# Performance work log

Hardware: AMD Instinct MI355X
Metric: run time of the kernel (lower is better)

Reference implementation:

```python
import jax, jax.numpy as jnp
import numpy as np

DIM = 2048
N_EXPERTS = 16
TOP_K = 4
MOE_INTER = 1024
SHARED_INTER = 2 * MOE_INTER  # n_shared_experts * moe_inter_dim
B, S = 4, 1024
INIT = 0.02


def setup_inputs() -> dict:
    key = jax.random.key(0)
    ks = jax.random.split(key, 8)
    return {
        "x": jax.random.normal(ks[0], (B, S, DIM), dtype=jnp.float32),
        "gate_w": jax.random.normal(ks[1], (DIM, N_EXPERTS), dtype=jnp.float32) * INIT,
        "w1": jax.random.normal(ks[2], (N_EXPERTS, DIM, MOE_INTER), dtype=jnp.float32) * INIT,
        "w2": jax.random.normal(ks[3], (N_EXPERTS, MOE_INTER, DIM), dtype=jnp.float32) * INIT,
        "w3": jax.random.normal(ks[4], (N_EXPERTS, DIM, MOE_INTER), dtype=jnp.float32) * INIT,
        "ws1": jax.random.normal(ks[5], (DIM, SHARED_INTER), dtype=jnp.float32) * INIT,
        "ws2": jax.random.normal(ks[6], (SHARED_INTER, DIM), dtype=jnp.float32) * INIT,
        "ws3": jax.random.normal(ks[7], (DIM, SHARED_INTER), dtype=jnp.float32) * INIT,
    }


def _moe_forward(x, gate_w, w1, w2, w3, ws1, ws2, ws3):
    shape = x.shape
    xf = x.reshape(-1, DIM)  # [T, D]
    # Gate: softmax scores, top-k selection (weights are the top-k probs)
    scores = jax.nn.softmax(xf @ gate_w, axis=-1)          # [T, E]
    weights, indices = jax.lax.top_k(scores, TOP_K)         # [T, K] each
    y = jnp.zeros_like(xf)
    # Fixed loop over experts (structural, not over data dims).
    for e in range(N_EXPERTS):
        # gate coefficient for expert e: 0 if not in token's top-k
        coef = jnp.sum(weights * (indices == e), axis=-1)   # [T]
        h = jax.nn.silu(xf @ w1[e]) * (xf @ w3[e])          # [T, I]
        y = y + coef[:, None] * (h @ w2[e])
    # Shared experts (always-on gated MLP)
    z = (jax.nn.silu(xf @ ws1) * (xf @ ws3)) @ ws2
    return (y + z).reshape(shape)


def reference(x, gate_w, w1, w2, w3, ws1, ws2, ws3):
    return _moe_forward(x, gate_w, w1, w2, w3, ws1, ws2, ws3)
```

## Files before the change

kernel.cpp:

```cpp
#include <hip/hip_runtime.h>
#include <hip/hip_bf16.h>
#include <stdint.h>

#define T_TOK 4096
#define DIMD  2048
#define NEXP  16
#define TOPK  4
#define NI    1024
#define NSH   2048
#define TCAP  320

typedef __attribute__((ext_vector_type(8))) short short8;
typedef __attribute__((ext_vector_type(4))) float f32x4;
typedef __attribute__((ext_vector_type(4))) unsigned short u16x4;
typedef __attribute__((ext_vector_type(8))) unsigned short u16x8;

__device__ __forceinline__ unsigned short f2bf(float f) {
    union { float f; unsigned u; } v; v.f = f;
    return (unsigned short)((v.u + 0x7fffu + ((v.u >> 16) & 1u)) >> 16);
}

__device__ __forceinline__ float bf2f(unsigned short b) {
    union { unsigned u; float f; } v; v.u = (unsigned)b << 16;
    return v.f;
}

__device__ __forceinline__ void gload16(const void* g, void* l) {
    __builtin_amdgcn_global_load_lds(
        (const __attribute__((address_space(1))) void*)g,
        (__attribute__((address_space(3))) void*)l, 16, 0, 0);
}

__global__ __launch_bounds__(256) void gwt_kernel(const float* __restrict__ gw,
                                                  float* __restrict__ gwT) {
    int i = blockIdx.x * 256 + threadIdx.x;
    int d = i >> 4, e = i & 15;
    gwT[e * DIMD + d] = gw[i];
}

__global__ __launch_bounds__(256) void gate_kernel(const float* __restrict__ x,
                                                   const float* __restrict__ gwT,
                                                   int* __restrict__ blk_cnt,
                                                   int* __restrict__ tk_er,
                                                   float* __restrict__ tk_wv,
                                                   unsigned short* __restrict__ xb) {
    __shared__ int h[16];
    const int blk = blockIdx.x;
    const int t = blk * 4 + (threadIdx.x >> 6);
    const int lane = threadIdx.x & 63;
    if (threadIdx.x < 16) h[threadIdx.x] = 0;
    __syncthreads();

    const f32x4* xr = (const f32x4*)(x + (size_t)t * DIMD);
    f32x4 xv[8];
#pragma unroll
    for (int i = 0; i < 8; ++i) xv[i] = xr[i * 64 + lane];

    {
        unsigned short* xo = xb + (size_t)t * DIMD;
#pragma unroll
        for (int i = 0; i < 8; ++i) {
            u16x4 o;
#pragma unroll
            for (int j = 0; j < 4; ++j) o[j] = f2bf(xv[i][j]);
            *(u16x4*)(xo + i * 256 + lane * 4) = o;
        }
    }

    float acc[NEXP];
#pragma unroll
    for (int e = 0; e < NEXP; ++e) {
        const f32x4* gr = (const f32x4*)(gwT + e * DIMD);
        float s = 0.f;
#pragma unroll
        for (int i = 0; i < 8; ++i) {
            f32x4 gv = gr[i * 64 + lane];
            s += xv[i][0] * gv[0] + xv[i][1] * gv[1] +
                 xv[i][2] * gv[2] + xv[i][3] * gv[3];
        }
        acc[e] = s;
    }
#pragma unroll
    for (int e = 0; e < NEXP; ++e) {
        float v = acc[e];
#pragma unroll
        for (int off = 32; off; off >>= 1) v += __shfl_xor(v, off, 64);
        acc[e] = v;
    }
    float m = acc[0];
#pragma unroll
    for (int e = 1; e < NEXP; ++e) m = fmaxf(m, acc[e]);
    float s = 0.f;
#pragma unroll
    for (int e = 0; e < NEXP; ++e) { acc[e] = expf(acc[e] - m); s += acc[e]; }
    float inv = 1.f / s;
#pragma unroll
    for (int e = 0; e < NEXP; ++e) acc[e] *= inv;

    float w4[TOPK]; int i4[TOPK];
#pragma unroll
    for (int k = 0; k < TOPK; ++k) {
        float bv = -1.f; int be = 0;
#pragma unroll
        for (int e = 0; e < NEXP; ++e)
            if (acc[e] > bv) { bv = acc[e]; be = e; }
        w4[k] = bv; i4[k] = be;
#pragma unroll
        for (int e = 0; e < NEXP; ++e)
            if (e == be) acc[e] = -1.f;
    }

    if (lane == 0) {
        int r4[TOPK];
#pragma unroll
        for (int k = 0; k < TOPK; ++k) r4[k] = atomicAdd(&h[i4[k]], 1);
#pragma unroll
        for (int k = 0; k < TOPK; ++k) {
            tk_er[t * 4 + k] = (i4[k] << 20) | r4[k];
            tk_wv[t * 4 + k] = w4[k];
        }
    }
    __syncthreads();
    if (threadIdx.x < 16) blk_cnt[blk * 16 + threadIdx.x] = h[threadIdx.x];
}

__global__ __launch_bounds__(256) void scan_kernel(const int* __restrict__ blk_cnt,
                                                   int* __restrict__ blk_off,
                                                   int* __restrict__ cnt,
                                                   int* __restrict__ offs,
                                                   int* __restrict__ table) {
    __shared__ int gsum[16][17];
    __shared__ int gbase[16][17];
    __shared__ int csh[16];
    int tid = threadIdx.x;
    int e = tid >> 4, g = tid & 15;
    {
        int s = 0;
        for (int b = g * 64; b < g * 64 + 64; ++b) s += blk_cnt[b * 16 + e];
        gsum[e][g] = s;
    }
    __syncthreads();
    if (tid < 16) {
        int run = 0;
        for (int g2 = 0; g2 < 16; ++g2) { gbase[tid][g2] = run; run += gsum[tid][g2]; }
        csh[tid] = run;
        cnt[tid] = run;
    }
    __syncthreads();
    {
        int run = gbase[e][g];
        for (int b = g * 64; b < g * 64 + 64; ++b) {
            blk_off[b * 16 + e] = run;
            run += blk_cnt[b * 16 + e];
        }
    }
    if (tid == 0) {
        int o = 0;
        for (int e2 = 0; e2 < 16; ++e2) { offs[e2] = o; o += csh[e2]; }
        offs[NEXP] = o;
    }
    __syncthreads();
    for (int idx = tid; idx < 8 * TCAP; idx += 256) {
        int c = idx & 7, j = idx >> 3;
        int n0 = ((csh[c] + 127) >> 7) << 3;
        int n1 = ((csh[c + 8] + 127) >> 7) << 3;
        int v = -1;
        if (j < n0)
            v = (c << 16) | ((j & 7) << 13) | ((j >> 3) * 128);
        else if (j < n0 + n1) {
            int j2 = j - n0;
            v = ((c + 8) << 16) | ((j2 & 7) << 13) | ((j2 >> 3) * 128);
        }
        table[idx] = v;
    }
}

__global__ __launch_bounds__(256) void fill_kernel(const int* __restrict__ tk_er,
                                                   const float* __restrict__ tk_wv,
                                                   const int* __restrict__ blk_off,
                                                   const int* __restrict__ offs,
                                                   int* __restrict__ list,
                                                   float* __restrict__ cw,
                                                   int* __restrict__ rows) {
    int i = blockIdx.x * 256 + threadIdx.x;
    int rec = tk_er[i];
    int e = rec >> 20, r = rec & 0xFFFFF;
    int t = i >> 2;
    int ro = blk_off[(t >> 2) * 16 + e] + r;
    list[e * T_TOK + ro] = t;
    cw[e * T_TOK + ro] = tk_wv[i];
    rows[i] = offs[e] + ro;
}

__global__ __launch_bounds__(256) void tq_pair(const float* __restrict__ s1,
                                               const float* __restrict__ s3,
                                               unsigned short* __restrict__ dst,
                                               int K, int N,
                                               size_t srcStrideE, size_t dstStrideE) {
    int e = blockIdx.z;
    s1 += (size_t)e * srcStrideE;
    s3 += (size_t)e * srcStrideE;
    dst += (size_t)e * dstStrideE;
    __shared__ unsigned short tile[64][72];
    const int t = threadIdx.x;
    const int k0 = blockIdx.y * 64, n0 = blockIdx.x * 64;
    const int lr = t >> 4, lc4 = (t & 15) * 4;
    const int sr8 = (t & 7) * 8, sn = t >> 3;
#pragma unroll
    for (int half = 0; half < 2; ++half) {
        const float* src = half ? s3 : s1;
#pragma unroll
        for (int r = 0; r < 4; ++r) {
            f32x4 v = *(const f32x4*)(src + (size_t)(k0 + lr + r * 16) * N + n0 + lc4);
#pragma unroll
            for (int j = 0; j < 4; ++j) tile[lr + r * 16][lc4 + j] = f2bf(v[j]);
        }
        __syncthreads();
#pragma unroll
        for (int q = 0; q < 2; ++q) {
            int nn = sn + q * 32;
            int n = n0 + nn;
            int rrow = (n >> 4) * 32 + half * 16 + (n & 15);
            u16x8 o;
#pragma unroll
            for (int j = 0; j < 8; ++j) o[j] = tile[sr8 + j][nn];
            *(u16x8*)(dst + (size_t)rrow * K + k0 + sr8) = o;
        }
        __syncthreads();
    }
}

__global__ __launch_bounds__(256) void tq_plain(const float* __restrict__ src,
                                                unsigned short* __restrict__ dst,
                                                int K, int N,
                                                size_t srcStrideE, size_t dstStrideE) {
    int e = blockIdx.z;
    src += (size_t)e * srcStrideE;
    dst += (size_t)e * dstStrideE;
    __shared__ unsigned short tile[64][72];
    const int t = threadIdx.x;
    const int k0 = blockIdx.y * 64, n0 = blockIdx.x * 64;
    const int lr = t >> 4, lc4 = (t & 15) * 4;
    const int sr8 = (t & 7) * 8, sn = t >> 3;
#pragma unroll
    for (int r = 0; r < 4; ++r) {
        f32x4 v = *(const f32x4*)(src + (size_t)(k0 + lr + r * 16) * N + n0 + lc4);
#pragma unroll
        for (int j = 0; j < 4; ++j) tile[lr + r * 16][lc4 + j] = f2bf(v[j]);
    }
    __syncthreads();
#pragma unroll
    for (int q = 0; q < 2; ++q) {
        int nn = sn + q * 32;
        int n = n0 + nn;
        u16x8 o;
#pragma unroll
        for (int j = 0; j < 8; ++j) o[j] = tile[sr8 + j][nn];
        *(u16x8*)(dst + (size_t)n * K + k0 + sr8) = o;
    }
}

__global__ __launch_bounds__(256) void gather_kernel(const unsigned short* __restrict__ dbuf,
                                                     const int* __restrict__ rows,
                                                     float* __restrict__ out) {
    const int t = blockIdx.x;
    const int c8 = threadIdx.x * 8;
    int r[4];
#pragma unroll
    for (int k = 0; k < 4; ++k) r[k] = rows[t * 4 + k];
    f32x4 a0, a1;
    {
        const f32x4* z = (const f32x4*)(out + (size_t)t * DIMD + c8);
        a0 = z[0]; a1 = z[1];
    }
#pragma unroll
    for (int k = 0; k < 4; ++k) {
        u16x8 d = *(const u16x8*)(dbuf + (size_t)r[k] * DIMD + c8);
#pragma unroll
        for (int j = 0; j < 4; ++j) { a0[j] += bf2f(d[j]); a1[j] += bf2f(d[4 + j]); }
    }
    f32x4* o = (f32x4*)(out + (size_t)t * DIMD + c8);
    o[0] = a0; o[1] = a1;
}

template <bool UP>
__global__ __launch_bounds__(512, 2) void gemm_f(
    const unsigned short* __restrict__ Ash, const unsigned short* __restrict__ Art,
    const unsigned short* __restrict__ Bsh, const unsigned short* __restrict__ Brt,
    const int* __restrict__ cnt, const int* __restrict__ offs,
    const int* __restrict__ list, const float* __restrict__ cw,
    unsigned short* __restrict__ hs, unsigned short* __restrict__ hbuf,
    float* __restrict__ fout, unsigned short* __restrict__ dbuf,
    const int* __restrict__ table) {
    constexpr int SHBLK = UP ? 512 : 256;

    const int bid = blockIdx.x;
    const bool routed = bid >= SHBLK;
    int bx, rb, e = 0, M, obase = 0;
    const unsigned short* Ap;
    const unsigned short* Bp;
    int ASTRr, BSTRr;
    if (!routed) {
        if (UP) { bx = bid & 15; rb = (bid >> 4) * 128; }
        else    { bx = bid >> 5; rb = (bid & 31) * 128; }
        M = T_TOK;
        Ap = Ash; Bp = Bsh;
        ASTRr = 2048; BSTRr = 2048;
    } else {
        int pk = table[bid - SHBLK];
        if (pk < 0) return;
        e = pk >> 16; bx = (pk >> 13) & 7; rb = pk & 8191;
        M = cnt[e]; obase = offs[e];
        Ap = Art;
        Bp = Brt + (UP ? (size_t)e * 2048 * 2048 : (size_t)e * 2048 * 1024);
        ASTRr = UP ? 2048 : 1024;
        BSTRr = UP ? 2048 : 1024;
    }
    const int NT = (!UP && routed) ? 32 : 64;

    extern __shared__ char smem[];

    const int tid = threadIdx.x;
    const int lane = tid & 63, wid = tid >> 6;
    const int wm = wid >> 2, wn = wid & 3;
    const int fr = lane & 15, fq = lane >> 4;
    const int offR = ((fr >> 1) << 7) + (((((fr & 1) << 2) | fq) ^ (fr >> 1)) << 4);
    const int d16 = tid * 16;

    const unsigned short* pA;
    const unsigned short* pB0;
    const unsigned short* pB1;
    {
        int c = tid, s = c >> 3, sl = (c & 7) ^ (s & 7);
        int rA = 2 * s + (sl >> 2), kk = (sl & 3) * 8;
        int gr = rb + rA;
        int cr = (gr < M) ? gr : (M - 1);
        size_t arow;
        if (!routed)  arow = (size_t)gr;
        else if (UP)  arow = (size_t)list[e * T_TOK + cr];
        else          arow = (size_t)(obase + cr);
        pA = Ap + arow * ASTRr + kk;
    }
#pragma unroll
    for (int u = 0; u < 2; ++u) {
        int c = u * 512 + tid, s = c >> 3, sl = (c & 7) ^ (s & 7);
        int rB = 2 * s + (sl >> 2), kk = (sl & 3) * 8;
        const unsigned short* p = Bp + (size_t)(bx * 256 + rB) * BSTRr + kk;
        if (u == 0) pB0 = p; else pB1 = p;
    }

    f32x4 acc[4][4];
#pragma unroll
    for (int m = 0; m < 4; ++m)
#pragma unroll
        for (int n = 0; n < 4; ++n) acc[m][n] = (f32x4)0.f;

    gload16(pA,      (void*)(smem + 0 + d16));
    gload16(pA + 32, (void*)(smem + 8192 + d16));
    gload16(pB0,      (void*)(smem + 24576 + d16));
    gload16(pB1,      (void*)(smem + 24576 + 8192 + d16));
    gload16(pB0 + 32, (void*)(smem + 24576 + 16384 + d16));
    gload16(pB1 + 32, (void*)(smem + 24576 + 16384 + 8192 + d16));
    pA += 64; pB0 += 64; pB1 += 64;
    asm volatile("s_waitcnt vmcnt(0)" ::: "memory");
    __builtin_amdgcn_s_barrier();

    int bA = 0, bA2 = 16384;
    int bB = 0, bB2 = 32768;
    for (int t = 0; t < NT; ++t) {
        short8 aF[4], bF[4];
#pragma unroll
        for (int m = 0; m < 4; ++m)
            aF[m] = *(const short8*)(smem + bA + wm * 4096 + m * 1024 + offR);
#pragma unroll
        for (int n = 0; n < 4; ++n)
            bF[n] = *(const short8*)(smem + 24576 + bB + wn * 4096 + n * 1024 + offR);
        const bool more = (t + 2 < NT);
        if (more) {
            gload16(pA, (void*)(smem + bA2 + d16));
            gload16(pB0, (void*)(smem + 24576 + bB2 + d16));
            gload16(pB1, (void*)(smem + 24576 + bB2 + 8192 + d16));
            pA += 32; pB0 += 32; pB1 += 32;
        }
        __builtin_amdgcn_s_setprio(1);
#pragma unroll
        for (int m = 0; m < 4; ++m)
#pragma unroll
            for (int n = 0; n < 4; ++n)
                acc[m][n] = __builtin_amdgcn_mfma_f32_16x16x32_bf16(aF[m], bF[n], acc[m][n], 0, 0, 0);
        __builtin_amdgcn_s_setprio(0);
        if (more) { asm volatile("s_waitcnt vmcnt(3)" ::: "memory"); }
        else      { asm volatile("s_waitcnt vmcnt(0)" ::: "memory"); }
        __builtin_amdgcn_s_barrier();
        bA = (bA == 16384) ? 0 : bA + 8192;
        bA2 = (bA2 == 16384) ? 0 : bA2 + 8192;
        bB = (bB == 32768) ? 0 : bB + 16384;
        bB2 = (bB2 == 32768) ? 0 : bB2 + 16384;
    }

    if constexpr (UP) {
        const int LDO = routed ? NI : NSH;
        unsigned short* hp = routed ? hbuf : hs;
#pragma unroll
        for (int m = 0; m < 4; ++m)
#pragma unroll
            for (int q = 0; q < 4; ++q) {
                int gr = rb + wm * 64 + m * 16 + fq * 4 + q;
                if (gr < M) {
                    float coef = routed ? cw[e * T_TOK + gr] : 1.f;
                    size_t orow = (size_t)((routed ? obase : 0) + gr) * LDO;
#pragma unroll
                    for (int nfp = 0; nfp < 2; ++nfp) {
                        float c1 = acc[m][2 * nfp][q], c3 = acc[m][2 * nfp + 1][q];
                        float h = c1 / (1.f + __expf(-c1)) * c3 * coef;
                        int ncol = (bx * 8 + wn * 2 + nfp) * 16 + fr;
                        hp[orow + ncol] = f2bf(h);
                    }
                }
            }
    } else {
#pragma unroll
        for (int m = 0; m < 4; ++m)
#pragma unroll
            for (int q = 0; q < 4; ++q) {
                int gr = rb + wm * 64 + m * 16 + fq * 4 + q;
                if (gr < M) {
                    if (routed) {
                        unsigned short* op = dbuf + (size_t)(obase + gr) * DIMD;
#pragma unroll
                        for (int nf = 0; nf < 4; ++nf) {
                            int col = bx * 256 + wn * 64 + nf * 16 + fr;
                            op[col] = f2bf(acc[m][nf][q]);
                        }
                    } else {
                        float* op = fout + (size_t)gr * DIMD;
#pragma unroll
                        for (int nf = 0; nf < 4; ++nf) {
                            int col = bx * 256 + wn * 64 + nf * 16 + fr;
                            op[col] = acc[m][nf][q];
                        }
                    }
                }
            }
    }
}

extern "C" void kernel_launch(void* const* d_in, const int* in_sizes, int n_in,
                              void* d_out, int out_size, void* d_ws, size_t ws_size,
                              hipStream_t stream) {
    const float* x   = (const float*)d_in[0];
    const float* gw  = (const float*)d_in[1];
    const float* w1  = (const float*)d_in[2];
    const float* w2  = (const float*)d_in[3];
    const float* w3  = (const float*)d_in[4];
    const float* ws1 = (const float*)d_in[5];
    const float* ws2 = (const float*)d_in[6];
    const float* ws3 = (const float*)d_in[7];
    float* out = (float*)d_out;

    char* p = (char*)d_ws;
    unsigned short* xb   = (unsigned short*)p; p += (size_t)T_TOK * DIMD * 2;
    unsigned short* hs   = (unsigned short*)p; p += (size_t)T_TOK * NSH * 2;
    unsigned short* hbuf = (unsigned short*)p; p += (size_t)T_TOK * TOPK * NI * 2;
    unsigned short* upT  = (unsigned short*)p; p += (size_t)NEXP * 2048 * DIMD * 2;
    unsigned short* w2T  = (unsigned short*)p; p += (size_t)NEXP * DIMD * NI * 2;
    unsigned short* upsT = (unsigned short*)p; p += (size_t)2 * NSH * DIMD * 2;
    unsigned short* ws2T = (unsigned short*)p; p += (size_t)DIMD * NSH * 2;
    float* gwT = (float*)p;                    p += (size_t)NEXP * DIMD * 4;
    float* cw = (float*)p;                     p += (size_t)NEXP * T_TOK * 4;
    int* list = (int*)p;                       p += (size_t)NEXP * T_TOK * 4;
    int* tk_er = (int*)p;                      p += (size_t)T_TOK * TOPK * 4;
    float* tk_wv = (float*)p;                  p += (size_t)T_TOK * TOPK * 4;
    int* rows = (int*)p;                       p += (size_t)T_TOK * TOPK * 4;
    int* blk_cnt = (int*)p;                    p += (size_t)1024 * 16 * 4;
    int* blk_off = (int*)p;                    p += (size_t)1024 * 16 * 4;
    int* cnt = (int*)p;                        p += 256;
    int* offs = (int*)p;                       p += 256;
    int* table = (int*)p;                      p += 4096 * 4;
    if ((size_t)(p - (char*)d_ws) > ws_size) return;
    unsigned short* dbuf = upT;

    hipFuncSetAttribute((const void*)&gemm_f<true>, hipFuncAttributeMaxDynamicSharedMemorySize, 73728);
    hipFuncSetAttribute((const void*)&gemm_f<false>, hipFuncAttributeMaxDynamicSharedMemorySize, 73728);

    gwt_kernel<<<(NEXP * DIMD) / 256, 256, 0, stream>>>(gw, gwT);
    gate_kernel<<<T_TOK / 4, 256, 0, stream>>>(x, gwT, blk_cnt, tk_er, tk_wv, xb);
    scan_kernel<<<1, 256, 0, stream>>>(blk_cnt, blk_off, cnt, offs, table);
    fill_kernel<<<T_TOK * TOPK / 256, 256, 0, stream>>>(tk_er, tk_wv, blk_off, offs,
                                                        list, cw, rows);

    tq_pair<<<dim3(NI / 64, DIMD / 64, NEXP), 256, 0, stream>>>(
        w1, w3, upT, DIMD, NI, (size_t)DIMD * NI, (size_t)2048 * DIMD);
    tq_pair<<<dim3(NSH / 64, DIMD / 64, 1), 256, 0, stream>>>(
        ws1, ws3, upsT, DIMD, NSH, 0, 0);
    tq_plain<<<dim3(DIMD / 64, NI / 64, NEXP), 256, 0, stream>>>(
        w2, w2T, NI, DIMD, (size_t)NI * DIMD, (size_t)DIMD * NI);
    tq_plain<<<dim3(DIMD / 64, NSH / 64, 1), 256, 0, stream>>>(
        ws2, ws2T, NSH, DIMD, 0, 0);

    gemm_f<true><<<512 + 8 * TCAP, 512, 73728, stream>>>(
        xb, xb, upsT, upT, cnt, offs, list, cw, hs, hbuf, nullptr, nullptr, table);
    gemm_f<false><<<256 + 8 * TCAP, 512, 73728, stream>>>(
        hs, hbuf, ws2T, w2T, cnt, offs, list, nullptr, nullptr, nullptr, out, dbuf, table);
    gather_kernel<<<T_TOK, 256, 0, stream>>>(dbuf, rows, out);
}
```

Before: 591.3 us.

## Enlarge GEMM tiles to 256x256 with K=64 steps and interleaved quadrant pipeline

Rewrites the fused grouped GEMM to compute 256x256 output tiles per block with a 64-wide K step, double-buffered in 128 KB of LDS. The main loop is split into four quadrant MFMA phases, with LDS reads and global-to-LDS loads interleaved between barriers. The routed tile table and block counts are rescaled to match. The goal is more data reuse per byte loaded and fewer blocks. The cost is one block per CU, more padding waste on small per-expert row counts, and more barriers per iteration.

```diff
diff --git a/kernel.cpp b/kernel.cpp
--- a/kernel.cpp
+++ b/kernel.cpp
@@ -8,7 +8,7 @@
 #define TOPK  4
 #define NI    1024
 #define NSH   2048
-#define TCAP  320
+#define TCAP  256
 
 typedef __attribute__((ext_vector_type(8))) short short8;
 typedef __attribute__((ext_vector_type(4))) float f32x4;
@@ -162,14 +162,14 @@
     __syncthreads();
     for (int idx = tid; idx < 8 * TCAP; idx += 256) {
         int c = idx & 7, j = idx >> 3;
-        int n0 = ((csh[c] + 127) >> 7) << 3;
-        int n1 = ((csh[c + 8] + 127) >> 7) << 3;
+        int n0 = ((csh[c] + 255) >> 8) << 3;
+        int n1 = ((csh[c + 8] + 255) >> 8) << 3;
         int v = -1;
         if (j < n0)
-            v = (c << 16) | ((j & 7) << 13) | ((j >> 3) * 128);
+            v = (c << 16) | ((j & 7) << 13) | ((j >> 3) * 256);
         else if (j < n0 + n1) {
             int j2 = j - n0;
-            v = ((c + 8) << 16) | ((j2 & 7) << 13) | ((j2 >> 3) * 128);
+            v = ((c + 8) << 16) | ((j2 & 7) << 13) | ((j2 >> 3) * 256);
         }
         table[idx] = v;
     }
@@ -283,6 +283,51 @@
     o[0] = a0; o[1] = a1;
 }
 
+
+#define BAR __builtin_amdgcn_s_barrier()
+#define LGKM0 do { asm volatile("s_waitcnt lgkmcnt(0)" ::: "memory"); \
+                   __builtin_amdgcn_sched_barrier(0); } while (0)
+
+#define SA(H, D, KT) do { \
+    gload16(pA[H][0] + (KT) * 64, (void*)(smem + (D) * 32768 + dofs[H][0])); \
+    gload16(pA[H][1] + (KT) * 64, (void*)(smem + (D) * 32768 + dofs[H][1])); \
+  } while (0)
+#define SB(H, D, KT) do { \
+    gload16(pB[H][0] + (KT) * 64, (void*)(smem + 65536 + (D) * 32768 + dofs[H][0])); \
+    gload16(pB[H][1] + (KT) * 64, (void*)(smem + 65536 + (D) * 32768 + dofs[H][1])); \
+  } while (0)
+
+#define RDA(MH, D) do { \
+    _Pragma("unroll") \
+    for (int m2 = 0; m2 < 4; ++m2) { \
+      const char* bp = smem + (D) * 32768 + wm * 16384 + ((MH) * 64 + m2 * 16 + fr) * 128; \
+      aF[m2][0] = *(const short8*)(bp + kA0); \
+      aF[m2][1] = *(const short8*)(bp + kA1); \
+    } } while (0)
+#define RDB(dst, NH, D) do { \
+    _Pragma("unroll") \
+    for (int n2 = 0; n2 < 2; ++n2) { \
+      const char* bp = smem + 65536 + (D) * 32768 + (wn >> 1) * 16384 + \
+                       ((wn & 1) * 64 + (NH) * 32 + n2 * 16 + fr) * 128; \
+      dst[n2][0] = *(const short8*)(bp + kA0); \
+      dst[n2][1] = *(const short8*)(bp + kA1); \
+    } } while (0)
+
+#define MM(MH, NH, BF) do { \
+    __builtin_amdgcn_s_setprio(1); \
+    _Pragma("unroll") \
+    for (int m2 = 0; m2 < 4; ++m2) { \
+      _Pragma("unroll") \
+      for (int n2 = 0; n2 < 2; ++n2) { \
+        acc[(MH) * 4 + m2][(NH) * 2 + n2] = __builtin_amdgcn_mfma_f32_16x16x32_bf16( \
+            aF[m2][0], BF[n2][0], acc[(MH) * 4 + m2][(NH) * 2 + n2], 0, 0, 0); \
+        acc[(MH) * 4 + m2][(NH) * 2 + n2] = __builtin_amdgcn_mfma_f32_16x16x32_bf16( \
+            aF[m2][1], BF[n2][1], acc[(MH) * 4 + m2][(NH) * 2 + n2], 0, 0, 0); \
+      } \
+    } \
+    __builtin_amdgcn_s_setprio(0); \
+  } while (0)
+
 template <bool UP>
 __global__ __launch_bounds__(512, 2) void gemm_f(
     const unsigned short* __restrict__ Ash, const unsigned short* __restrict__ Art,
@@ -292,7 +337,7 @@
     unsigned short* __restrict__ hs, unsigned short* __restrict__ hbuf,
     float* __restrict__ fout, unsigned short* __restrict__ dbuf,
     const int* __restrict__ table) {
-    constexpr int SHBLK = UP ? 512 : 256;
+    constexpr int SHBLK = UP ? 256 : 128;
 
     const int bid = blockIdx.x;
     const bool routed = bid >= SHBLK;
@@ -301,8 +346,8 @@
     const unsigned short* Bp;
     int ASTRr, BSTRr;
     if (!routed) {
-        if (UP) { bx = bid & 15; rb = (bid >> 4) * 128; }
-        else    { bx = bid >> 5; rb = (bid & 31) * 128; }
+        if (UP) { bx = bid & 15; rb = (bid >> 4) * 256; }
+        else    { bx = bid >> 4; rb = (bid & 15) * 256; }
         M = T_TOK;
         Ap = Ash; Bp = Bsh;
         ASTRr = 2048; BSTRr = 2048;
@@ -316,7 +361,7 @@
         ASTRr = UP ? 2048 : 1024;
         BSTRr = UP ? 2048 : 1024;
     }
-    const int NT = (!UP && routed) ? 32 : 64;
+    const int NT = UP ? 32 : (routed ? 16 : 32);
 
     extern __shared__ char smem[];
 
@@ -324,120 +369,111 @@
     const int lane = tid & 63, wid = tid >> 6;
     const int wm = wid >> 2, wn = wid & 3;
     const int fr = lane & 15, fq = lane >> 4;
-    const int offR = ((fr >> 1) << 7) + (((((fr & 1) << 2) | fq) ^ (fr >> 1)) << 4);
-    const int d16 = tid * 16;
-
-    const unsigned short* pA;
-    const unsigned short* pB0;
-    const unsigned short* pB1;
-    {
-        int c = tid, s = c >> 3, sl = (c & 7) ^ (s & 7);
-        int rA = 2 * s + (sl >> 2), kk = (sl & 3) * 8;
-        int gr = rb + rA;
-        int cr = (gr < M) ? gr : (M - 1);
-        size_t arow;
-        if (!routed)  arow = (size_t)gr;
-        else if (UP)  arow = (size_t)list[e * T_TOK + cr];
-        else          arow = (size_t)(obase + cr);
-        pA = Ap + arow * ASTRr + kk;
-    }
-#pragma unroll
-    for (int u = 0; u < 2; ++u) {
-        int c = u * 512 + tid, s = c >> 3, sl = (c & 7) ^ (s & 7);
-        int rB = 2 * s + (sl >> 2), kk = (sl & 3) * 8;
-        const unsigned short* p = Bp + (size_t)(bx * 256 + rB) * BSTRr + kk;
-        if (u == 0) pB0 = p; else pB1 = p;
-    }
-
-    f32x4 acc[4][4];
-#pragma unroll
-    for (int m = 0; m < 4; ++m)
+    const int s7 = fr & 7;
+    const int kA0 = ((fq ^ s7) << 4);
+    const int kA1 = kA0 ^ 64;
+
+    const unsigned short* pA[2][2];
+    const unsigned short* pB[2][2];
+    int dofs[2][2];
+#pragma unroll
+    for (int h = 0; h < 2; ++h)
+#pragma unroll
+        for (int i = 0; i < 2; ++i) {
+            int c = i * 512 + tid;
+            int lr = c >> 3;
+            int lsl = (c & 7) ^ (lr & 7);
+            dofs[h][i] = h * 16384 + c * 16;
+            int grA = rb + h * 128 + lr;
+            int crA = (grA < M) ? grA : (M - 1);
+            size_t arow;
+            if (!routed)  arow = (size_t)grA;
+            else if (UP)  arow = (size_t)list[e * T_TOK + crA];
+            else          arow = (size_t)(obase + crA);
+            pA[h][i] = Ap + arow * ASTRr + lsl * 8;
+            pB[h][i] = Bp + (size_t)(bx * 256 + h * 128 + lr) * BSTRr + lsl * 8;
+        }
+
+    f32x4 acc[8][4];
+#pragma unroll
+    for (int m = 0; m < 8; ++m)
 #pragma unroll
         for (int n = 0; n < 4; ++n) acc[m][n] = (f32x4)0.f;
 
-    gload16(pA,      (void*)(smem + 0 + d16));
-    gload16(pA + 32, (void*)(smem + 8192 + d16));
-    gload16(pB0,      (void*)(smem + 24576 + d16));
-    gload16(pB1,      (void*)(smem + 24576 + 8192 + d16));
-    gload16(pB0 + 32, (void*)(smem + 24576 + 16384 + d16));
-    gload16(pB1 + 32, (void*)(smem + 24576 + 16384 + 8192 + d16));
-    pA += 64; pB0 += 64; pB1 += 64;
-    asm volatile("s_waitcnt vmcnt(0)" ::: "memory");
-    __builtin_amdgcn_s_barrier();
-
-    int bA = 0, bA2 = 16384;
-    int bB = 0, bB2 = 32768;
+    short8 aF[4][2], bF0[2][2], bF1[2][2];
+
+    SB(0, 0, 0); SB(1, 0, 0); SA(0, 0, 0); SA(1, 0, 0);
+    SB(0, 1, 1); SA(0, 1, 1);
+    asm volatile("s_waitcnt vmcnt(4)" ::: "memory");
+    BAR;
+
     for (int t = 0; t < NT; ++t) {
-        short8 aF[4], bF[4];
-#pragma unroll
-        for (int m = 0; m < 4; ++m)
-            aF[m] = *(const short8*)(smem + bA + wm * 4096 + m * 1024 + offR);
-#pragma unroll
-        for (int n = 0; n < 4; ++n)
-            bF[n] = *(const short8*)(smem + 24576 + bB + wn * 4096 + n * 1024 + offR);
-        const bool more = (t + 2 < NT);
-        if (more) {
-            gload16(pA, (void*)(smem + bA2 + d16));
-            gload16(pB0, (void*)(smem + 24576 + bB2 + d16));
-            gload16(pB1, (void*)(smem + 24576 + bB2 + 8192 + d16));
-            pA += 32; pB0 += 32; pB1 += 32;
-        }
-        __builtin_amdgcn_s_setprio(1);
-#pragma unroll
-        for (int m = 0; m < 4; ++m)
-#pragma unroll
-            for (int n = 0; n < 4; ++n)
-                acc[m][n] = __builtin_amdgcn_mfma_f32_16x16x32_bf16(aF[m], bF[n], acc[m][n], 0, 0, 0);
-        __builtin_amdgcn_s_setprio(0);
-        if (more) { asm volatile("s_waitcnt vmcnt(3)" ::: "memory"); }
-        else      { asm volatile("s_waitcnt vmcnt(0)" ::: "memory"); }
-        __builtin_amdgcn_s_barrier();
-        bA = (bA == 16384) ? 0 : bA + 8192;
-        bA2 = (bA2 == 16384) ? 0 : bA2 + 8192;
-        bB = (bB == 32768) ? 0 : bB + 16384;
-        bB2 = (bB2 == 32768) ? 0 : bB2 + 16384;
+        const int D = t & 1;
+        const bool m1 = (t + 1 < NT), m2g = (t + 2 < NT);
+        RDA(0, D); RDB(bF0, 0, D);
+        if (m1) SB(1, D ^ 1, t + 1);
+        BAR; LGKM0;
+        MM(0, 0, bF0);
+        BAR;
+        RDB(bF1, 1, D);
+        if (m1) SA(1, D ^ 1, t + 1);
+        BAR; LGKM0;
+        MM(0, 1, bF1);
+        BAR;
+        RDA(1, D);
+        if (m2g) SB(0, D, t + 2);
+        BAR; LGKM0;
+        MM(1, 1, bF1);
+        BAR;
+        if (m2g) SA(0, D, t + 2);
+        MM(1, 0, bF0);
+        if (m1) {
+            if (m2g) { asm volatile("s_waitcnt vmcnt(4)" ::: "memory"); }
+            else     { asm volatile("s_waitcnt vmcnt(0)" ::: "memory"); }
+        }
+        BAR;
     }
 
     if constexpr (UP) {
         const int LDO = routed ? NI : NSH;
         unsigned short* hp = routed ? hbuf : hs;
 #pragma unroll
-        for (int m = 0; m < 4; ++m)
+        for (int m = 0; m < 8; ++m)
 #pragma unroll
             for (int q = 0; q < 4; ++q) {
-                int gr = rb + wm * 64 + m * 16 + fq * 4 + q;
+                int gr = rb + wm * 128 + (m >> 2) * 64 + (m & 3) * 16 + fq * 4 + q;
                 if (gr < M) {
                     float coef = routed ? cw[e * T_TOK + gr] : 1.f;
                     size_t orow = (size_t)((routed ? obase : 0) + gr) * LDO;
 #pragma unroll
-                    for (int nfp = 0; nfp < 2; ++nfp) {
-                        float c1 = acc[m][2 * nfp][q], c3 = acc[m][2 * nfp + 1][q];
-                        float h = c1 / (1.f + __expf(-c1)) * c3 * coef;
-                        int ncol = (bx * 8 + wn * 2 + nfp) * 16 + fr;
-                        hp[orow + ncol] = f2bf(h);
+                    for (int j = 0; j < 2; ++j) {
+                        float c1 = acc[m][2 * j][q], c3 = acc[m][2 * j + 1][q];
+                        float hv = c1 / (1.f + __expf(-c1)) * c3 * coef;
+                        int ncol = (bx * 8 + wn * 2 + j) * 16 + fr;
+                        hp[orow + ncol] = f2bf(hv);
                     }
                 }
             }
     } else {
 #pragma unroll
-        for (int m = 0; m < 4; ++m)
+        for (int m = 0; m < 8; ++m)
 #pragma unroll
             for (int q = 0; q < 4; ++q) {
-                int gr = rb + wm * 64 + m * 16 + fq * 4 + q;
+                int gr = rb + wm * 128 + (m >> 2) * 64 + (m & 3) * 16 + fq * 4 + q;
                 if (gr < M) {
                     if (routed) {
                         unsigned short* op = dbuf + (size_t)(obase + gr) * DIMD;
 #pragma unroll
-                        for (int nf = 0; nf < 4; ++nf) {
-                            int col = bx * 256 + wn * 64 + nf * 16 + fr;
-                            op[col] = f2bf(acc[m][nf][q]);
+                        for (int n = 0; n < 4; ++n) {
+                            int col = bx * 256 + wn * 64 + (n >> 1) * 32 + (n & 1) * 16 + fr;
+                            op[col] = f2bf(acc[m][n][q]);
                         }
                     } else {
                         float* op = fout + (size_t)gr * DIMD;
 #pragma unroll
-                        for (int nf = 0; nf < 4; ++nf) {
-                            int col = bx * 256 + wn * 64 + nf * 16 + fr;
-                            op[col] = acc[m][nf][q];
+                        for (int n = 0; n < 4; ++n) {
+                            int col = bx * 256 + wn * 64 + (n >> 1) * 32 + (n & 1) * 16 + fr;
+                            op[col] = acc[m][n][q];
                         }
                     }
                 }
@@ -476,12 +512,12 @@
     int* blk_off = (int*)p;                    p += (size_t)1024 * 16 * 4;
     int* cnt = (int*)p;                        p += 256;
     int* offs = (int*)p;                       p += 256;
-    int* table = (int*)p;                      p += 4096 * 4;
+    int* table = (int*)p;                      p += 8192 * 4;
     if ((size_t)(p - (char*)d_ws) > ws_size) return;
     unsigned short* dbuf = upT;
 
-    hipFuncSetAttribute((const void*)&gemm_f<true>, hipFuncAttributeMaxDynamicSharedMemorySize, 73728);
-    hipFuncSetAttribute((const void*)&gemm_f<false>, hipFuncAttributeMaxDynamicSharedMemorySize, 73728);
+    hipFuncSetAttribute((const void*)&gemm_f<true>, hipFuncAttributeMaxDynamicSharedMemorySize, 131072);
+    hipFuncSetAttribute((const void*)&gemm_f<false>, hipFuncAttributeMaxDynamicSharedMemorySize, 131072);
 
     gwt_kernel<<<(NEXP * DIMD) / 256, 256, 0, stream>>>(gw, gwT);
     gate_kernel<<<T_TOK / 4, 256, 0, stream>>>(x, gwT, blk_cnt, tk_er, tk_wv, xb);
@@ -498,9 +534,9 @@
     tq_plain<<<dim3(DIMD / 64, NSH / 64, 1), 256, 0, stream>>>(
         ws2, ws2T, NSH, DIMD, 0, 0);
 
-    gemm_f<true><<<512 + 8 * TCAP, 512, 73728, stream>>>(
+    gemm_f<true><<<256 + 8 * TCAP, 512, 131072, stream>>>(
         xb, xb, upsT, upT, cnt, offs, list, cw, hs, hbuf, nullptr, nullptr, table);
-    gemm_f<false><<<256 + 8 * TCAP, 512, 73728, stream>>>(
+    gemm_f<false><<<128 + 8 * TCAP, 512, 131072, stream>>>(
         hs, hbuf, ws2T, w2T, cnt, offs, list, nullptr, nullptr, nullptr, out, dbuf, table);
     gather_kernel<<<T_TOK, 256, 0, stream>>>(dbuf, rows, out);
 }
```

New measurement: 585.9 us. Within noise of the previous version (-0.9%).
